# Kernel tuning notes

Hardware: AMD Instinct MI355X
Metric: run time of the kernel (lower is better)

Reference implementation:

```python
import jax, jax.numpy as jnp
import numpy as np

E = 1024  # embedding_dim
D = 1024  # output_dim

def setup_inputs() -> dict:
    key = jax.random.key(0)
    k_x, k_q, k_k, k_v = jax.random.split(key, 4)
    embeddings = jax.random.normal(k_x, (4, 2048, E), dtype=jnp.float32)
    scale = 1.0 / np.sqrt(E)
    Wq = jax.random.normal(k_q, (E, D), dtype=jnp.float32) * scale
    Wk = jax.random.normal(k_k, (E, D), dtype=jnp.float32) * scale
    Wv = jax.random.normal(k_v, (E, D), dtype=jnp.float32) * scale
    return {"embeddings": embeddings, "Wq": Wq, "Wk": Wk, "Wv": Wv}

def reference(embeddings, Wq, Wk, Wv):
    # QKV projections (no bias, qkv_bias=False)
    q = jnp.einsum('bse,ed->bsd', embeddings, Wq)
    k = jnp.einsum('bse,ed->bsd', embeddings, Wk)
    v = jnp.einsum('bse,ed->bsd', embeddings, Wv)
    n = embeddings.shape[1]
    scores = jnp.einsum('bqd,bkd->bqk', q, k)  # [B, S, S]
    causal = jnp.tril(jnp.ones((n, n), dtype=bool))  # mask upper triangle (diag=1)
    scores = jnp.where(causal, scores, -jnp.inf)
    scale = jnp.asarray(k.shape[-1], scores.dtype) ** 0.5
    weights = jax.nn.softmax(scores / scale, axis=-1)
    # dropout p=0.0 -> identity
    context = jnp.einsum('bqk,bkd->bqd', weights, v)
    return context
```

## Files before the change

### kernel.cpp

```cpp
#include <hip/hip_runtime.h>

typedef unsigned short u16;
typedef __attribute__((ext_vector_type(8))) short short8;
typedef __attribute__((ext_vector_type(4))) float f32x4;
typedef __attribute__((ext_vector_type(4))) unsigned short u16x4;
typedef __attribute__((ext_vector_type(4))) float float4v;

__device__ __forceinline__ u16 f2bf(float f) {
  union { float f; unsigned u; } v; v.f = f;
  unsigned r = v.u + 0x7FFFu + ((v.u >> 16) & 1u);
  return (u16)(r >> 16);
}

__device__ __forceinline__ void gload16(const void* g, void* l) {
  __builtin_amdgcn_global_load_lds(
      (const __attribute__((address_space(1))) unsigned int*)g,
      (__attribute__((address_space(3))) unsigned int*)l, 16, 0, 0);
}

__global__ __launch_bounds__(256) void kconv(const float* __restrict__ X,
                                             const float* __restrict__ Wq,
                                             const float* __restrict__ Wk,
                                             const float* __restrict__ Wv,
                                             u16* __restrict__ Xb,
                                             u16* __restrict__ Wt) {
  __shared__ float tile[32][33];
  const int bx = blockIdx.x;
  if (bx < 8192) {
    size_t i = ((size_t)bx * 256 + threadIdx.x) * 4;
    float4v v = *(const float4v*)(X + i);
    u16x4 o;
    o.x = f2bf(v.x); o.y = f2bf(v.y); o.z = f2bf(v.z); o.w = f2bf(v.w);
    *(u16x4*)(Xb + i) = o;
  } else {
    const int l = bx - 8192;
    const int z = l >> 10;
    const int rem = l & 1023;
    const int n0 = (rem & 31) * 32, k0 = (rem >> 5) * 32;
    const float* W = z == 0 ? Wq : (z == 1 ? Wk : Wv);
    u16* O = Wt + (size_t)z * 1024 * 1024;
    const int tx = threadIdx.x & 31, ty = threadIdx.x >> 5;
#pragma unroll
    for (int r = 0; r < 32; r += 8)
      tile[ty + r][tx] = W[(size_t)(k0 + ty + r) * 1024 + n0 + tx];
    __syncthreads();
#pragma unroll
    for (int r = 0; r < 32; r += 8)
      O[(size_t)(n0 + ty + r) * 1024 + k0 + tx] = f2bf(tile[tx][ty + r]);
  }
}

__device__ __forceinline__ void stage64(const u16* __restrict__ pan, int ld,
                                        int k0, u16* dst, int t) {
  const int rb = t >> 3;
  const int sw = ((t & 7) ^ (rb & 7)) * 8;
  const int ds = (t & 7) * 8;
#pragma unroll
  for (int j = 0; j < 4; ++j) {
    const int row = j * 32 + rb;
    gload16(pan + (size_t)row * ld + k0 + sw, dst + row * 64 + ds);
  }
}

__device__ __forceinline__ void gemm64(const u16* __restrict__ A,
                                       const u16* __restrict__ B,
                                       int lda, int ldb,
                                       int rowBase, int colBase, int kIters,
                                       u16* As, u16* Bs, f32x4 acc[4][4]) {
  const int t = threadIdx.x;
  const int wid = t >> 6, lane = t & 63;
  const int wm = wid >> 1, wn = wid & 1;
  const int l15 = lane & 15;
  const int sw = l15 & 7;
  const int sl = lane >> 4;
  const int s0 = ((sl    ) ^ sw) * 8;
  const int s1 = ((sl + 4) ^ sw) * 8;
  const u16* ga = A + (size_t)rowBase * lda;
  const u16* gb = B + (size_t)colBase * ldb;

  for (int kt = 0; kt < kIters; ++kt) {
    const int k0 = kt * 64;
    stage64(ga, lda, k0, As, t);
    stage64(gb, ldb, k0, Bs, t);
    __syncthreads();
#pragma unroll
    for (int h = 0; h < 2; ++h) {
      const int so = h ? s1 : s0;
      short8 a[4], b[4];
#pragma unroll
      for (int mi = 0; mi < 4; mi++)
        a[mi] = *(const short8*)(As + (wm * 64 + mi * 16 + l15) * 64 + so);
#pragma unroll
      for (int ni = 0; ni < 4; ni++)
        b[ni] = *(const short8*)(Bs + (wn * 64 + ni * 16 + l15) * 64 + so);
#pragma unroll
      for (int mi = 0; mi < 4; mi++)
#pragma unroll
        for (int ni = 0; ni < 4; ni++)
          acc[mi][ni] = __builtin_amdgcn_mfma_f32_16x16x32_bf16(
              a[mi], b[ni], acc[mi][ni], 0, 0, 0);
    }
    __syncthreads();
  }
}

__global__ __launch_bounds__(256, 3) void kqkv(const u16* __restrict__ Xb,
                                               const u16* __restrict__ Wt,
                                               u16* __restrict__ Qb,
                                               u16* __restrict__ Kb,
                                               u16* __restrict__ Vt) {
  __shared__ __align__(16) u16 As[128 * 64];
  __shared__ __align__(16) u16 Bs[128 * 64];
  const f32x4 z4 = {0.f, 0.f, 0.f, 0.f};
  f32x4 acc[4][4];
#pragma unroll
  for (int i = 0; i < 4; i++)
#pragma unroll
    for (int j = 0; j < 4; j++) acc[i][j] = z4;

  const int l = blockIdx.x;
  const int xcd = l & 7, idx = l >> 3;
  const int cz = idx >> 3, rloc = idx & 7;
  const int rowTile = xcd * 8 + rloc;
  const int z = cz >> 3, colTile = cz & 7;

  const int rowBase = rowTile * 128, colBase = colTile * 128;
  const u16* Bt = Wt + (size_t)z * 1024 * 1024;
  gemm64(Xb, Bt, 1024, 1024, rowBase, colBase, 16, As, Bs, acc);

  const int t = threadIdx.x, wid = t >> 6, lane = t & 63;
  const int wm = wid >> 1, wn = wid & 1;
  const int r0 = rowBase + wm * 64 + ((lane >> 4) * 4);
  const int c0 = colBase + wn * 64 + (lane & 15);
  if (z < 2) {
    u16* O = z ? Kb : Qb;
#pragma unroll
    for (int mi = 0; mi < 4; mi++) {
      int r = r0 + mi * 16;
#pragma unroll
      for (int ni = 0; ni < 4; ni++) {
        int c = c0 + ni * 16;
#pragma unroll
        for (int j = 0; j < 4; j++)
          O[(size_t)(r + j) * 1024 + c] = f2bf(acc[mi][ni][j]);
      }
    }
  } else {
#pragma unroll
    for (int mi = 0; mi < 4; mi++) {
      int s0r = r0 + mi * 16;
      int bb = s0r >> 11, sl = s0r & 2047;
#pragma unroll
      for (int ni = 0; ni < 4; ni++) {
        int d = c0 + ni * 16;
        u16x4 pk;
        pk.x = f2bf(acc[mi][ni][0]);
        pk.y = f2bf(acc[mi][ni][1]);
        pk.z = f2bf(acc[mi][ni][2]);
        pk.w = f2bf(acc[mi][ni][3]);
        *(u16x4*)(Vt + ((size_t)bb * 1024 + d) * 2048 + sl) = pk;
      }
    }
  }
}

__global__ __launch_bounds__(256, 3) void kscores(const u16* __restrict__ Q,
                                                  const u16* __restrict__ K,
                                                  float* __restrict__ Sc) {
  const int x = blockIdx.x, b = blockIdx.y;
  const int xcd = x & 7, idx = x >> 3;
  const int tid = xcd * 17 + idx;
  int tr = (int)((sqrtf(8.f * tid + 1.f) - 1.f) * 0.5f);
  while ((tr + 1) * (tr + 2) / 2 <= tid) ++tr;
  while (tr * (tr + 1) / 2 > tid) --tr;
  const int tc = tid - tr * (tr + 1) / 2;

  __shared__ __align__(16) u16 As[128 * 64];
  __shared__ __align__(16) u16 Bs[128 * 64];
  const f32x4 z4 = {0.f, 0.f, 0.f, 0.f};
  f32x4 acc[4][4];
#pragma unroll
  for (int i = 0; i < 4; i++)
#pragma unroll
    for (int j = 0; j < 4; j++) acc[i][j] = z4;

  const u16* Qp = Q + (size_t)b * 2048 * 1024;
  const u16* Kp = K + (size_t)b * 2048 * 1024;
  gemm64(Qp, Kp, 1024, 1024, tr * 128, tc * 128, 16, As, Bs, acc);

  float* S = Sc + (size_t)b * 2048 * 2048;
  const int t = threadIdx.x, wid = t >> 6, lane = t & 63;
  const int wm = wid >> 1, wn = wid & 1;
  const int r0 = tr * 128 + wm * 64 + ((lane >> 4) * 4);
  const int c0 = tc * 128 + wn * 64 + (lane & 15);
#pragma unroll
  for (int mi = 0; mi < 4; mi++) {
    int r = r0 + mi * 16;
#pragma unroll
    for (int ni = 0; ni < 4; ni++) {
      int c = c0 + ni * 16;
#pragma unroll
      for (int j = 0; j < 4; j++)
        S[(size_t)(r + j) * 2048 + c] = acc[mi][ni][j] * 0.03125f;
    }
  }
}

__global__ __launch_bounds__(256) void ksoftmax(const float* __restrict__ Sc,
                                                u16* __restrict__ P) {
  const int i = blockIdx.x, b = blockIdx.y;
  const int nv = i + 1;
  const int nceil = ((i >> 7) + 1) << 7;
  const float* S = Sc + ((size_t)b * 2048 + i) * 2048;
  u16* Pr = P + ((size_t)b * 2048 + i) * 2048;
  __shared__ float srow[2048];
  __shared__ float red[4];
  const int t = threadIdx.x, lane = t & 63, wid = t >> 6;

  float lm = -3.0e38f;
  for (int j = t; j < nv; j += 256) {
    float v = S[j];
    srow[j] = v;
    lm = fmaxf(lm, v);
  }
#pragma unroll
  for (int o = 32; o > 0; o >>= 1) lm = fmaxf(lm, __shfl_down(lm, o));
  if (lane == 0) red[wid] = lm;
  __syncthreads();
  const float m = fmaxf(fmaxf(red[0], red[1]), fmaxf(red[2], red[3]));

  float ls = 0.f;
  for (int j = t; j < nv; j += 256) {
    float e = __expf(srow[j] - m);
    srow[j] = e;
    ls += e;
  }
#pragma unroll
  for (int o = 32; o > 0; o >>= 1) ls += __shfl_down(ls, o);
  __syncthreads();
  if (lane == 0) red[wid] = ls;
  __syncthreads();
  const float inv = 1.f / (red[0] + red[1] + red[2] + red[3]);

  for (int j = t; j < nv; j += 256) Pr[j] = f2bf(srow[j] * inv);
  for (int j = nv + t; j < nceil; j += 256) Pr[j] = 0;
}

__global__ __launch_bounds__(256, 3) void kpv(const u16* __restrict__ P,
                                              const u16* __restrict__ Vt,
                                              float* __restrict__ Out) {
  const int x = blockIdx.x, b = blockIdx.y;
  const int xcd = x & 7, idx = x >> 3;
  const int tr = (idx < 8) ? xcd : (15 - xcd);
  const int col = idx & 7;

  __shared__ __align__(16) u16 As[128 * 64];
  __shared__ __align__(16) u16 Bs[128 * 64];
  const f32x4 z4 = {0.f, 0.f, 0.f, 0.f};
  f32x4 acc[4][4];
#pragma unroll
  for (int i = 0; i < 4; i++)
#pragma unroll
    for (int j = 0; j < 4; j++) acc[i][j] = z4;

  const u16* Pp = P + (size_t)b * 2048 * 2048;
  const u16* Vp = Vt + (size_t)b * 1024 * 2048;
  gemm64(Pp, Vp, 2048, 2048, tr * 128, col * 128, (tr + 1) * 2, As, Bs, acc);

  float* Ob = Out + (size_t)b * 2048 * 1024;
  const int t = threadIdx.x, wid = t >> 6, lane = t & 63;
  const int wm = wid >> 1, wn = wid & 1;
  const int r0 = tr * 128 + wm * 64 + ((lane >> 4) * 4);
  const int c0 = col * 128 + wn * 64 + (lane & 15);
#pragma unroll
  for (int mi = 0; mi < 4; mi++) {
    int r = r0 + mi * 16;
#pragma unroll
    for (int ni = 0; ni < 4; ni++) {
      int c = c0 + ni * 16;
#pragma unroll
      for (int j = 0; j < 4; j++)
        Ob[(size_t)(r + j) * 1024 + c] = acc[mi][ni][j];
    }
  }
}

extern "C" void kernel_launch(void* const* d_in, const int* in_sizes, int n_in,
                              void* d_out, int out_size, void* d_ws,
                              size_t ws_size, hipStream_t stream) {
  const float* X = (const float*)d_in[0];
  const float* Wq = (const float*)d_in[1];
  const float* Wk = (const float*)d_in[2];
  const float* Wv = (const float*)d_in[3];
  float* Out = (float*)d_out;

  char* ws = (char*)d_ws;
  u16* Xb = (u16*)(ws);
  u16* Wt = (u16*)(ws + 16777216);
  u16* Qb = (u16*)(ws + 23068672);
  u16* Kb = (u16*)(ws + 39845888);
  u16* Vt = (u16*)(ws + 56623104);
  float* Sc = (float*)(ws + 73400320);
  u16* P = (u16*)(ws + 140509184);

  kconv<<<11264, 256, 0, stream>>>(X, Wq, Wk, Wv, Xb, Wt);
  kqkv<<<1536, 256, 0, stream>>>(Xb, Wt, Qb, Kb, Vt);
  kscores<<<dim3(136, 4), 256, 0, stream>>>(Qb, Kb, Sc);
  ksoftmax<<<dim3(2048, 4), 256, 0, stream>>>(Sc, P);
  kpv<<<dim3(128, 4), 256, 0, stream>>>(P, Vt, Out);
}
```

Baseline: 147.7 us.

## Store attention scores in fp16 and vectorize softmax over full rows

The score kernel now writes scaled scores as fp16 instead of fp32, halving the bytes written to the intermediate score buffer. The softmax kernel is restructured so each thread loads 8 fp16 values with one vector load, keeps them in registers instead of staging through shared memory, masks by causal index, and writes the full bf16 probability row with one vector store. Each row is now read and written across its full width rather than only up to the causal boundary. Masked entries get a tiny nonzero probability from the clamped exponent, and scores lose precision in fp16.

```diff
diff --git a/kernel.cpp b/kernel.cpp
--- a/kernel.cpp
+++ b/kernel.cpp
@@ -1,4 +1,5 @@
 #include <hip/hip_runtime.h>
+#include <hip/hip_fp16.h>
 
 typedef unsigned short u16;
 typedef __attribute__((ext_vector_type(8))) short short8;
@@ -10,6 +11,16 @@
   union { float f; unsigned u; } v; v.f = f;
   unsigned r = v.u + 0x7FFFu + ((v.u >> 16) & 1u);
   return (u16)(r >> 16);
+}
+
+__device__ __forceinline__ u16 f2h(float f) {
+  __half h = __float2half(f);
+  return *reinterpret_cast<u16*>(&h);
+}
+
+__device__ __forceinline__ float h2f(u16 b) {
+  __half_raw hr; hr.x = b;
+  return __half2float(__half(hr));
 }
 
 __device__ __forceinline__ void gload16(const void* g, void* l) {
@@ -166,7 +177,7 @@
 
 __global__ __launch_bounds__(256, 3) void kscores(const u16* __restrict__ Q,
                                                   const u16* __restrict__ K,
-                                                  float* __restrict__ Sc) {
+                                                  u16* __restrict__ Sch) {
   const int x = blockIdx.x, b = blockIdx.y;
   const int xcd = x & 7, idx = x >> 3;
   const int tid = xcd * 17 + idx;
@@ -188,7 +199,7 @@
   const u16* Kp = K + (size_t)b * 2048 * 1024;
   gemm64(Qp, Kp, 1024, 1024, tr * 128, tc * 128, 16, As, Bs, acc);
 
-  float* S = Sc + (size_t)b * 2048 * 2048;
+  u16* S = Sch + (size_t)b * 2048 * 2048;
   const int t = threadIdx.x, wid = t >> 6, lane = t & 63;
   const int wm = wid >> 1, wn = wid & 1;
   const int r0 = tr * 128 + wm * 64 + ((lane >> 4) * 4);
@@ -201,49 +212,51 @@
       int c = c0 + ni * 16;
 #pragma unroll
       for (int j = 0; j < 4; j++)
-        S[(size_t)(r + j) * 2048 + c] = acc[mi][ni][j] * 0.03125f;
-    }
-  }
-}
-
-__global__ __launch_bounds__(256) void ksoftmax(const float* __restrict__ Sc,
+        S[(size_t)(r + j) * 2048 + c] = f2h(acc[mi][ni][j] * 0.03125f);
+    }
+  }
+}
+
+__global__ __launch_bounds__(256) void ksoftmax(const u16* __restrict__ Sch,
                                                 u16* __restrict__ P) {
   const int i = blockIdx.x, b = blockIdx.y;
-  const int nv = i + 1;
-  const int nceil = ((i >> 7) + 1) << 7;
-  const float* S = Sc + ((size_t)b * 2048 + i) * 2048;
-  u16* Pr = P + ((size_t)b * 2048 + i) * 2048;
-  __shared__ float srow[2048];
+  const int t = threadIdx.x, lane = t & 63, wid = t >> 6;
   __shared__ float red[4];
-  const int t = threadIdx.x, lane = t & 63, wid = t >> 6;
-
-  float lm = -3.0e38f;
-  for (int j = t; j < nv; j += 256) {
-    float v = S[j];
-    srow[j] = v;
-    lm = fmaxf(lm, v);
-  }
+
+  const size_t rowoff = ((size_t)b * 2048 + i) * 2048 + t * 8;
+  short8 raw = *(const short8*)(Sch + rowoff);
+  const int base = t * 8;
+  float v[8];
+#pragma unroll
+  for (int k = 0; k < 8; ++k)
+    v[k] = (base + k <= i) ? h2f((u16)raw[k]) : -3.0e38f;
+
+  float lm = v[0];
+#pragma unroll
+  for (int k = 1; k < 8; ++k) lm = fmaxf(lm, v[k]);
 #pragma unroll
   for (int o = 32; o > 0; o >>= 1) lm = fmaxf(lm, __shfl_down(lm, o));
   if (lane == 0) red[wid] = lm;
   __syncthreads();
   const float m = fmaxf(fmaxf(red[0], red[1]), fmaxf(red[2], red[3]));
-
-  float ls = 0.f;
-  for (int j = t; j < nv; j += 256) {
-    float e = __expf(srow[j] - m);
-    srow[j] = e;
-    ls += e;
+  __syncthreads();
+
+  float e[8], ls = 0.f;
+#pragma unroll
+  for (int k = 0; k < 8; ++k) {
+    e[k] = __expf(fmaxf(v[k] - m, -88.f));
+    ls += e[k];
   }
 #pragma unroll
   for (int o = 32; o > 0; o >>= 1) ls += __shfl_down(ls, o);
-  __syncthreads();
   if (lane == 0) red[wid] = ls;
   __syncthreads();
   const float inv = 1.f / (red[0] + red[1] + red[2] + red[3]);
 
-  for (int j = t; j < nv; j += 256) Pr[j] = f2bf(srow[j] * inv);
-  for (int j = nv + t; j < nceil; j += 256) Pr[j] = 0;
+  short8 out;
+#pragma unroll
+  for (int k = 0; k < 8; ++k) out[k] = (short)f2bf(e[k] * inv);
+  *(short8*)(P + rowoff) = out;
 }
 
 __global__ __launch_bounds__(256, 3) void kpv(const u16* __restrict__ P,
@@ -300,12 +313,12 @@
   u16* Qb = (u16*)(ws + 23068672);
   u16* Kb = (u16*)(ws + 39845888);
   u16* Vt = (u16*)(ws + 56623104);
-  float* Sc = (float*)(ws + 73400320);
+  u16* Sch = (u16*)(ws + 73400320);
   u16* P = (u16*)(ws + 140509184);
 
   kconv<<<11264, 256, 0, stream>>>(X, Wq, Wk, Wv, Xb, Wt);
   kqkv<<<1536, 256, 0, stream>>>(Xb, Wt, Qb, Kb, Vt);
-  kscores<<<dim3(136, 4), 256, 0, stream>>>(Qb, Kb, Sc);
-  ksoftmax<<<dim3(2048, 4), 256, 0, stream>>>(Sc, P);
+  kscores<<<dim3(136, 4), 256, 0, stream>>>(Qb, Kb, Sch);
+  ksoftmax<<<dim3(2048, 4), 256, 0, stream>>>(Sch, P);
   kpv<<<dim3(128, 4), 256, 0, stream>>>(P, Vt, Out);
 }
```

Result: faster. 140.8 us (-4.7%).
